# Optimization experiments

Measured on AMD Instinct MI355X. Metric: run time of the kernel, lower is better.

Reference implementation:

```python
import jax, jax.numpy as jnp
import numpy as np

B, C, T = 8, 512, 1024
EXP = 2
E = EXP * C          # 1024, gate/value width
H, HD = 8, 64        # heads, qk head dim
QK = H * HD          # 512
AVG_LEN = 512
EPS = 1e-5


def setup_inputs() -> dict:
    key = jax.random.key(0)
    ks = jax.random.split(key, 10)
    s = 0.02
    return {
        "x": jax.random.normal(ks[0], (B, C, T), jnp.float32),
        "W_in": jax.random.normal(ks[1], (2 * E, C), jnp.float32) * s,
        "b_in": jnp.zeros((2 * E,), jnp.float32),
        "W_attn": jax.random.normal(ks[2], (QK, C), jnp.float32) * s,
        "b_attn": jnp.zeros((QK,), jnp.float32),
        "w_q": 1.0 + jax.random.normal(ks[3], (QK,), jnp.float32) * 0.1,
        "b_q": jax.random.normal(ks[4], (QK,), jnp.float32) * 0.1,
        "w_k": 1.0 + jax.random.normal(ks[5], (QK,), jnp.float32) * 0.1,
        "b_k": jax.random.normal(ks[6], (QK,), jnp.float32) * 0.1,
        "W_out": jax.random.normal(ks[7], (C, E), jnp.float32) * s,
        "b_out": jnp.zeros((C,), jnp.float32),
        "gamma": jnp.ones((C,), jnp.float32),
    }


def reference(x, W_in, b_in, W_attn, b_attn, w_q, b_q, w_k, b_k, W_out, b_out, gamma):
    residual = x
    # mlp_in (1x1 conv) + SiLU, then chunk into gate u and value v, each (B,E,T)
    uv = jax.nn.silu(jnp.einsum('oc,bct->bot', W_in, x) + b_in[:, None])
    u, v = uv[:, :E], uv[:, E:]
    # mlp_attn (1x1 conv); no activation (activation_attn unused in forward)
    z = jnp.einsum('oc,bct->bot', W_attn, x) + b_attn[:, None]  # (B,QK,T)
    # depthwise 1x1 conv on cat(z,z) = two independent per-channel affines
    q = z * w_q[:, None] + b_q[:, None]
    k = z * w_k[:, None] + b_k[:, None]
    # split heads: q,k -> (B,H,T,HD); v -> (B,H,T,E//H)
    q = q.reshape(B, H, HD, T).transpose(0, 1, 3, 2)
    k = k.reshape(B, H, HD, T).transpose(0, 1, 3, 2)
    vh = v.reshape(B, H, E // H, T).transpose(0, 1, 3, 2)
    # entropy-invariant scale: (log n / log avg_len) / sqrt(d)
    scale = (np.log(T) / np.log(AVG_LEN)) / np.sqrt(HD)
    scores = jnp.einsum('bhqd,bhkd->bhqk', q, k) * jnp.float32(scale)
    attn = jax.nn.softmax(scores, axis=-1)
    o = jnp.einsum('bhqk,bhke->bhqe', attn, vh)        # (B,H,T,E//H)
    o = o.transpose(0, 1, 3, 2).reshape(B, E, T)       # back to (B,E,T)
    # gate, project out, residual + RMSNorm over channel dim
    out = jnp.einsum('ce,bet->bct', W_out, u * o) + b_out[:, None]
    y = residual + out
    rms = jax.lax.rsqrt(jnp.mean(y * y, axis=1, keepdims=True) + EPS)
    return y * rms * gamma[:, None]
```

## Files before the change

kernel.cpp:

```cpp
#include <hip/hip_runtime.h>

typedef __attribute__((ext_vector_type(8))) short short8;
typedef __attribute__((ext_vector_type(4))) float f32x4;
typedef __attribute__((ext_vector_type(16))) float f32x16;

__device__ __forceinline__ unsigned short f2b(float f) {
  union { float f; unsigned u; } x; x.f = f;
  unsigned r = (x.u + 0x7fffu + ((x.u >> 16) & 1u)) >> 16;
  return (unsigned short)r;
}
__device__ __forceinline__ float b2f(unsigned short b) {
  union { unsigned u; float f; } x; x.u = ((unsigned)b) << 16;
  return x.f;
}
__device__ __forceinline__ unsigned cvtpk(float lo, float hi) {
  unsigned r;
  asm("v_cvt_pk_bf16_f32 %0, %1, %2" : "=v"(r) : "v"(lo), "v"(hi));
  return r;
}
__device__ __forceinline__ void plswap(unsigned& a, unsigned& b) {
  asm volatile("v_permlane32_swap_b32 %0, %1" : "+v"(a), "+v"(b));
}

#define GLDS16(gp, lp)                                                                  \
  __builtin_amdgcn_global_load_lds((const __attribute__((address_space(1))) void*)(gp), \
                                   (__attribute__((address_space(3))) void*)(lp), 16, 0, 0)

__global__ void prep_w_kernel(const float* __restrict__ W_in, const float* __restrict__ W_attn,
                              const float* __restrict__ W_out, unsigned short* __restrict__ Wcat,
                              unsigned short* __restrict__ WoutB) {
  const int n1 = 2048 * 512, n2 = 512 * 512, n3 = 512 * 1024;
  for (int i = blockIdx.x * 256 + threadIdx.x; i < n1 + n2 + n3; i += gridDim.x * 256) {
    if (i < n1) Wcat[i] = f2b(W_in[i]);
    else if (i < n1 + n2) Wcat[i] = f2b(W_attn[i - n1]);
    else WoutB[i - n1 - n2] = f2b(W_out[i - n1 - n2]);
  }
}

__global__ __launch_bounds__(256) void transpose_x_kernel(const float* __restrict__ x,
                                                          unsigned short* __restrict__ xT) {
  __shared__ float tile[32][33];
  const int bid = blockIdx.x;
  const int b = bid >> 9;
  const int rem = bid & 511;
  const int c0 = (rem >> 5) << 5;
  const int t0 = (rem & 31) << 5;
  const int tj = threadIdx.x & 31, ti = threadIdx.x >> 5;
#pragma unroll
  for (int r = 0; r < 32; r += 8)
    tile[ti + r][tj] = x[(((size_t)b << 9) + c0 + ti + r) * 1024 + t0 + tj];
  __syncthreads();
#pragma unroll
  for (int r = 0; r < 32; r += 8)
    xT[(((size_t)b << 10) + t0 + ti + r) * 512 + c0 + tj] = f2b(tile[tj][ti + r]);
}

__device__ __forceinline__ void gemm_stage(const unsigned short* Ag, const unsigned short* Bg,
                                           int lda, int ldb, int k0, unsigned short* lsA,
                                           unsigned short* lsB, int buf, int sr, int sk,
                                           int ldst) {
  const int bb = buf * 8192;
  GLDS16(Ag + (size_t)sr * lda + k0 + sk, (char*)lsA + bb + ldst);
  GLDS16(Ag + (size_t)(sr + 64) * lda + k0 + sk, (char*)lsA + bb + 4096 + ldst);
  GLDS16(Bg + (size_t)sr * ldb + k0 + sk, (char*)lsB + bb + ldst);
  GLDS16(Bg + (size_t)(sr + 64) * ldb + k0 + sk, (char*)lsB + bb + 4096 + ldst);
}

__device__ __forceinline__ void gemm_bt_core(const unsigned short* __restrict__ Ag,
                                             const unsigned short* __restrict__ Bg, int lda,
                                             int ldb, int K, unsigned short* lsA,
                                             unsigned short* lsB, f32x4 acc[4][4]) {
  const int tid = threadIdx.x;
  const int lane = tid & 63;
  const int w = tid >> 6;
  const int wr = w >> 1, wc = w & 1;
  const int sr = tid >> 2;
  const int sk = (tid & 3) << 3;
  const int ldst = (tid >> 6) << 10;

  const int nt = K >> 5;
  gemm_stage(Ag, Bg, lda, ldb, 0, lsA, lsB, 0, sr, sk, ldst);
  for (int t = 0; t < nt; ++t) {
    const int cur = t & 1;
    if (t + 1 < nt) {
      gemm_stage(Ag, Bg, lda, ldb, (t + 1) << 5, lsA, lsB, cur ^ 1, sr, sk, ldst);
      asm volatile("s_waitcnt vmcnt(4)" ::: "memory");
    } else {
      asm volatile("s_waitcnt vmcnt(0)" ::: "memory");
    }
    __builtin_amdgcn_s_barrier();
    short8 af[4], bfr[4];
    const int bb = cur * 8192;
    const int ko = (lane >> 4) << 4;
    const int ra = (wr << 6) + (lane & 15);
    const int rb = (wc << 6) + (lane & 15);
#pragma unroll
    for (int mi = 0; mi < 4; ++mi)
      af[mi] = *(const short8*)((const char*)lsA + bb + ((ra + (mi << 4)) << 6) + ko);
#pragma unroll
    for (int ni = 0; ni < 4; ++ni)
      bfr[ni] = *(const short8*)((const char*)lsB + bb + ((rb + (ni << 4)) << 6) + ko);
#pragma unroll
    for (int mi = 0; mi < 4; ++mi)
#pragma unroll
      for (int ni = 0; ni < 4; ++ni)
        acc[mi][ni] =
            __builtin_amdgcn_mfma_f32_16x16x32_bf16(af[mi], bfr[ni], acc[mi][ni], 0, 0, 0);
    __builtin_amdgcn_s_barrier();
  }
}

__global__ __launch_bounds__(256) void gemm_a_kernel(
    const unsigned short* __restrict__ Wcat, const unsigned short* __restrict__ xT,
    const float* __restrict__ b_in, const float* __restrict__ b_attn,
    const float* __restrict__ w_q, const float* __restrict__ b_q, const float* __restrict__ w_k,
    const float* __restrict__ b_k, unsigned short* __restrict__ u, unsigned short* __restrict__ v,
    unsigned short* __restrict__ qT, unsigned short* __restrict__ kT) {
  __shared__ __align__(16) unsigned short lsA[16384];
  __shared__ __align__(16) unsigned short lsB[16384];
  const int bid = ((blockIdx.x & 7) * 160) + (blockIdx.x >> 3);
  const int b = bid / 160;
  const int rem = bid % 160;
  const int m0 = (rem >> 3) << 7;
  const int n0 = (rem & 7) << 7;
  f32x4 acc[4][4];
  const f32x4 z4 = {0.f, 0.f, 0.f, 0.f};
#pragma unroll
  for (int mi = 0; mi < 4; ++mi)
#pragma unroll
    for (int ni = 0; ni < 4; ++ni) acc[mi][ni] = z4;

  const unsigned short* Ag = Wcat + (size_t)m0 * 512;
  const unsigned short* Bg = xT + ((size_t)b << 19) + ((size_t)n0 << 9);
  gemm_bt_core(Ag, Bg, 512, 512, 512, lsA, lsB, acc);

  const int lane = threadIdx.x & 63;
  const int w = threadIdx.x >> 6;
  const int wr = w >> 1, wc = w & 1;
#pragma unroll
  for (int mi = 0; mi < 4; ++mi) {
    const int row0 = m0 + (wr << 6) + (mi << 4) + ((lane >> 4) << 2);
#pragma unroll
    for (int ni = 0; ni < 4; ++ni) {
      const int col = n0 + (wc << 6) + (ni << 4) + (lane & 15);
      if (row0 < 2048) {
#pragma unroll
        for (int i = 0; i < 4; ++i) {
          const int row = row0 + i;
          const float s = acc[mi][ni][i] + b_in[row];
          const float r = s / (1.f + __expf(-s));
          if (row < 1024)
            u[((((size_t)b << 10) + row) << 10) + col] = f2b(r);
          else
            v[((((size_t)b << 10) + (row - 1024)) << 10) + col] = f2b(r);
        }
      } else {
        const int c0 = row0 - 2048;
        ushort4 qv, kv;
        unsigned short* qp = (unsigned short*)&qv;
        unsigned short* kp = (unsigned short*)&kv;
#pragma unroll
        for (int i = 0; i < 4; ++i) {
          const int c = c0 + i;
          const float z = acc[mi][ni][i] + b_attn[c];
          qp[i] = f2b(z * w_q[c] + b_q[c]);
          kp[i] = f2b(z * w_k[c] + b_k[c]);
        }
        const int h = c0 >> 6, d = c0 & 63;
        const size_t base = ((((size_t)b * 8 + h) << 10) + col) * 64 + d;
        *(ushort4*)(qT + base) = qv;
        *(ushort4*)(kT + base) = kv;
      }
    }
  }
}

__global__ __launch_bounds__(512, 4) void attn_kernel(const unsigned short* __restrict__ qT,
                                                      const unsigned short* __restrict__ kT,
                                                      const unsigned short* __restrict__ v,
                                                      const unsigned short* __restrict__ u,
                                                      unsigned short* __restrict__ uoT) {
  __shared__ __align__(16) unsigned short Kls[2][4096];
  __shared__ __align__(16) unsigned short Vls[2][8192];
  const float SCALE = 0.13888888888888889f;
  const int bx = blockIdx.x;
  const int xcd = bx & 7, idx = bx >> 3;
  const int bh = (xcd << 3) + (idx & 7);
  const int qb = idx >> 3;
  const int b = bh >> 3, h = bh & 7;
  const int tid = threadIdx.x;
  const int lane = tid & 63;
  const int w = tid >> 6;
  const int l5 = lane >> 5;
  const int l31 = lane & 31;
  const int qw = w >> 1, eh = w & 1;
  const int q0 = qb << 7;

  const unsigned short* qh = qT + ((size_t)bh << 16);
  const unsigned short* kh = kT + ((size_t)bh << 16);
  const unsigned short* vh = v + ((((size_t)b << 10) + (h << 7)) << 10);

  short8 qf[4];
#pragma unroll
  for (int ds = 0; ds < 4; ++ds)
    qf[ds] = *(const short8*)(qh + (size_t)(q0 + (qw << 5) + l31) * 64 + (ds << 4) + (l5 << 3));

  f32x16 o[2];
#pragma unroll
  for (int eb = 0; eb < 2; ++eb)
#pragma unroll
    for (int i = 0; i < 16; ++i) o[eb][i] = 0.f;
  float lacc = 0.f;

  const int srow = tid >> 3;
  const int scol = (((tid & 7) ^ (srow & 7)) << 3);

#define ATTN_STAGE(buf, kt)                                                        \
  {                                                                                \
    const int t2 = (kt) << 6;                                                      \
    GLDS16(kh + (size_t)(t2 + srow) * 64 + scol, (char*)Kls[buf] + (w << 10));     \
    GLDS16(vh + ((size_t)srow << 10) + t2 + scol, (char*)Vls[buf] + (w << 10));    \
    GLDS16(vh + ((size_t)(64 + srow) << 10) + t2 + scol,                           \
           (char*)Vls[buf] + 8192 + (w << 10));                                    \
  }

  ATTN_STAGE(0, 0);
  union U8 { short8 s8; unsigned u4[4]; };
  for (int kt = 0; kt < 16; ++kt) {
    const int cur = kt & 1;
    if (kt < 15) {
      ATTN_STAGE(cur ^ 1, kt + 1);
      asm volatile("s_waitcnt vmcnt(3)" ::: "memory");
    } else {
      asm volatile("s_waitcnt vmcnt(0)" ::: "memory");
    }
    __builtin_amdgcn_s_barrier();

    const char* kb = (const char*)Kls[cur];
    const char* vb = (const char*)Vls[cur];
    U8 pf[4];

    {
      f32x16 s;
#pragma unroll
      for (int i = 0; i < 16; ++i) s[i] = 0.f;
      const int kr = l31;
      __builtin_amdgcn_s_setprio(1);
#pragma unroll
      for (int ds = 0; ds < 4; ++ds) {
        short8 kf = *(const short8*)(kb + (kr << 7) +
                                     (((ds << 5) + (l5 << 4)) ^ ((kr & 7) << 4)));
        s = __builtin_amdgcn_mfma_f32_32x32x16_bf16(kf, qf[ds], s, 0, 0, 0);
      }
      __builtin_amdgcn_s_setprio(0);
      float p[16];
#pragma unroll
      for (int i = 0; i < 16; ++i) {
        p[i] = __expf(s[i] * SCALE);
        lacc += p[i];
      }
      unsigned W00 = cvtpk(p[0], p[1]), W01 = cvtpk(p[2], p[3]);
      unsigned W10 = cvtpk(p[4], p[5]), W11 = cvtpk(p[6], p[7]);
      unsigned W20 = cvtpk(p[8], p[9]), W21 = cvtpk(p[10], p[11]);
      unsigned W30 = cvtpk(p[12], p[13]), W31 = cvtpk(p[14], p[15]);
      unsigned a = W10, bq = W00; plswap(a, bq);
      pf[0].u4[0] = bq; pf[0].u4[2] = a;
      unsigned c = W11, d = W01; plswap(c, d);
      pf[0].u4[1] = d; pf[0].u4[3] = c;
      unsigned e = W30, f = W20; plswap(e, f);
      pf[1].u4[0] = f; pf[1].u4[2] = e;
      unsigned g = W31, hh = W21; plswap(g, hh);
      pf[1].u4[1] = hh; pf[1].u4[3] = g;
    }
    {
      f32x16 s;
#pragma unroll
      for (int i = 0; i < 16; ++i) s[i] = 0.f;
      const int kr = 32 + l31;
      __builtin_amdgcn_s_setprio(1);
#pragma unroll
      for (int ds = 0; ds < 4; ++ds) {
        short8 kf = *(const short8*)(kb + (kr << 7) +
                                     (((ds << 5) + (l5 << 4)) ^ ((kr & 7) << 4)));
        s = __builtin_amdgcn_mfma_f32_32x32x16_bf16(kf, qf[ds], s, 0, 0, 0);
      }
      __builtin_amdgcn_s_setprio(0);
      float p[16];
#pragma unroll
      for (int i = 0; i < 16; ++i) {
        p[i] = __expf(s[i] * SCALE);
        lacc += p[i];
      }
      unsigned W00 = cvtpk(p[0], p[1]), W01 = cvtpk(p[2], p[3]);
      unsigned W10 = cvtpk(p[4], p[5]), W11 = cvtpk(p[6], p[7]);
      unsigned W20 = cvtpk(p[8], p[9]), W21 = cvtpk(p[10], p[11]);
      unsigned W30 = cvtpk(p[12], p[13]), W31 = cvtpk(p[14], p[15]);
      unsigned a = W10, bq = W00; plswap(a, bq);
      pf[2].u4[0] = bq; pf[2].u4[2] = a;
      unsigned c = W11, d = W01; plswap(c, d);
      pf[2].u4[1] = d; pf[2].u4[3] = c;
      unsigned e = W30, f = W20; plswap(e, f);
      pf[3].u4[0] = f; pf[3].u4[2] = e;
      unsigned g = W31, hh = W21; plswap(g, hh);
      pf[3].u4[1] = hh; pf[3].u4[3] = g;
    }

    __builtin_amdgcn_s_setprio(1);
#pragma unroll
    for (int eb = 0; eb < 2; ++eb) {
      const int vrow = (eh << 6) + (eb << 5) + l31;
#pragma unroll
      for (int ks = 0; ks < 4; ++ks) {
        short8 vf = *(const short8*)(vb + (vrow << 7) +
                                     (((ks << 5) + (l5 << 4)) ^ ((vrow & 7) << 4)));
        o[eb] = __builtin_amdgcn_mfma_f32_32x32x16_bf16(vf, pf[ks].s8, o[eb], 0, 0, 0);
      }
    }
    __builtin_amdgcn_s_setprio(0);
    __builtin_amdgcn_s_barrier();
  }
#undef ATTN_STAGE

  lacc += __shfl_xor(lacc, 32, 64);
  const float rl = 1.f / lacc;
  const int t = q0 + (qw << 5) + l31;

#pragma unroll
  for (int eb = 0; eb < 2; ++eb) {
#pragma unroll
    for (int a = 0; a < 4; ++a) {
      const int e4 = (eh << 6) + (eb << 5) + (a << 3) + (l5 << 2);
      const int eg = (h << 7) + e4;
      ushort4 outv;
      unsigned short* op = (unsigned short*)&outv;
#pragma unroll
      for (int j = 0; j < 4; ++j) {
        const int i = (a << 2) + j;
        const float oo = o[eb][i] * rl;
        const float uu = b2f(u[((((size_t)b << 10) + eg + j) << 10) + t]);
        op[j] = f2b(oo * uu);
      }
      *(ushort4*)(uoT + ((((size_t)b << 10) + t) << 10) + eg) = outv;
    }
  }
}

__global__ __launch_bounds__(256) void gemm_c_kernel(const unsigned short* __restrict__ uoT,
                                                     const unsigned short* __restrict__ WoutB,
                                                     const float* __restrict__ x,
                                                     const float* __restrict__ b_out,
                                                     float* __restrict__ y) {
  __shared__ __align__(16) unsigned short lsA[16384];
  __shared__ __align__(16) unsigned short lsB[16384];
  const int bid = ((blockIdx.x & 7) * 32) + (blockIdx.x >> 3);
  const int b = bid >> 5;
  const int rem = bid & 31;
  const int m0 = (rem >> 2) << 7;
  const int n0 = (rem & 3) << 7;
  f32x4 acc[4][4];
  const f32x4 z4 = {0.f, 0.f, 0.f, 0.f};
#pragma unroll
  for (int mi = 0; mi < 4; ++mi)
#pragma unroll
    for (int ni = 0; ni < 4; ++ni) acc[mi][ni] = z4;

  const unsigned short* Ag = uoT + ((size_t)b << 20) + ((size_t)m0 << 10);
  const unsigned short* Bg = WoutB + ((size_t)n0 << 10);
  gemm_bt_core(Ag, Bg, 1024, 1024, 1024, lsA, lsB, acc);

  const int lane = threadIdx.x & 63;
  const int w = threadIdx.x >> 6;
  const int wr = w >> 1, wc = w & 1;
#pragma unroll
  for (int mi = 0; mi < 4; ++mi) {
    const int t4 = m0 + (wr << 6) + (mi << 4) + ((lane >> 4) << 2);
#pragma unroll
    for (int ni = 0; ni < 4; ++ni) {
      const int c = n0 + (wc << 6) + (ni << 4) + (lane & 15);
      const size_t base = ((((size_t)b << 9) + c) << 10) + t4;
      const f32x4 xv = *(const f32x4*)(x + base);
      const float bo = b_out[c];
      f32x4 o;
#pragma unroll
      for (int i = 0; i < 4; ++i) o[i] = acc[mi][ni][i] + bo + xv[i];
      *(f32x4*)(y + base) = o;
    }
  }
}

__global__ __launch_bounds__(256) void rms_kernel(const float* __restrict__ y,
                                                  const float* __restrict__ gamma,
                                                  float* __restrict__ out) {
  __shared__ float part[8][32];
  __shared__ float rmsv[32];
  const int bid = blockIdx.x;
  const int b = bid >> 5;
  const int t0 = (bid & 31) << 5;
  const int tid = threadIdx.x;
  const int tt = tid & 31, cg = tid >> 5;
  const int t = t0 + tt;
  float vals[64];
  float ss = 0.f;
#pragma unroll
  for (int ci = 0; ci < 64; ++ci) {
    const int c = (cg << 6) + ci;
    const float vv = y[((((size_t)b << 9) + c) << 10) + t];
    vals[ci] = vv;
    ss += vv * vv;
  }
  part[cg][tt] = ss;
  __syncthreads();
  if (tid < 32) {
    float tot = 0.f;
#pragma unroll
    for (int g = 0; g < 8; ++g) tot += part[g][tid];
    rmsv[tid] = rsqrtf(tot / 512.f + 1e-5f);
  }
  __syncthreads();
  const float rm = rmsv[tt];
#pragma unroll
  for (int ci = 0; ci < 64; ++ci) {
    const int c = (cg << 6) + ci;
    out[((((size_t)b << 9) + c) << 10) + t] = vals[ci] * rm * gamma[c];
  }
}

extern "C" void kernel_launch(void* const* d_in, const int* in_sizes, int n_in, void* d_out,
                              int out_size, void* d_ws, size_t ws_size, hipStream_t stream) {
  const float* x = (const float*)d_in[0];
  const float* W_in = (const float*)d_in[1];
  const float* b_in = (const float*)d_in[2];
  const float* W_attn = (const float*)d_in[3];
  const float* b_attn = (const float*)d_in[4];
  const float* w_q = (const float*)d_in[5];
  const float* b_q = (const float*)d_in[6];
  const float* w_k = (const float*)d_in[7];
  const float* b_k = (const float*)d_in[8];
  const float* W_out = (const float*)d_in[9];
  const float* b_out = (const float*)d_in[10];
  const float* gamma = (const float*)d_in[11];
  float* out = (float*)d_out;

  char* ws = (char*)d_ws;
  size_t off = 0;
  auto alloc = [&](size_t bytes) {
    char* p = ws + off;
    off += (bytes + 255) & ~(size_t)255;
    return p;
  };
  unsigned short* Wcat = (unsigned short*)alloc((size_t)2560 * 512 * 2);
  unsigned short* WoutB = (unsigned short*)alloc((size_t)512 * 1024 * 2);
  unsigned short* xT = (unsigned short*)alloc((size_t)8 * 1024 * 512 * 2);
  unsigned short* u = (unsigned short*)alloc((size_t)8 * 1024 * 1024 * 2);
  unsigned short* v = (unsigned short*)alloc((size_t)8 * 1024 * 1024 * 2);
  unsigned short* qT = (unsigned short*)alloc((size_t)8 * 8 * 1024 * 64 * 2);
  unsigned short* kT = (unsigned short*)alloc((size_t)8 * 8 * 1024 * 64 * 2);
  unsigned short* uoT = (unsigned short*)alloc((size_t)8 * 1024 * 1024 * 2);
  float* y = (float*)alloc((size_t)8 * 512 * 1024 * 4);
  if (off > ws_size) return;

  prep_w_kernel<<<896, 256, 0, stream>>>(W_in, W_attn, W_out, Wcat, WoutB);
  transpose_x_kernel<<<4096, 256, 0, stream>>>(x, xT);
  gemm_a_kernel<<<1280, 256, 0, stream>>>(Wcat, xT, b_in, b_attn, w_q, b_q, w_k, b_k, u, v, qT,
                                          kT);
  attn_kernel<<<512, 512, 0, stream>>>(qT, kT, v, u, uoT);
  gemm_c_kernel<<<256, 256, 0, stream>>>(uoT, WoutB, x, b_out, y);
  rms_kernel<<<256, 256, 0, stream>>>(y, gamma, out);
}
```

Before: 145.4 us.

## Widen gemm_a tile to 128x256 with 512 threads and trim LDS buffers

The input-projection GEMM now uses 512-thread blocks, each computing a 128x256 output tile with a 2x4 wave layout. Each 256-column tile sits inside one batch, so 640 blocks cover all outputs instead of 1280, and every weight tile loaded from global memory is reused across twice as many columns. The shared buffers are resized to match, and gemm_c's LDS arrays are shrunk to the 16 KB each that gemm_bt_core actually uses, which could raise occupancy. The cost is fewer blocks in flight for gemm_a and a different load and wait pattern per stage.

```diff
diff --git a/kernel.cpp b/kernel.cpp
--- a/kernel.cpp
+++ b/kernel.cpp
@@ -55,74 +55,28 @@
     xT[(((size_t)b << 10) + t0 + ti + r) * 512 + c0 + tj] = f2b(tile[tj][ti + r]);
 }
 
-__device__ __forceinline__ void gemm_stage(const unsigned short* Ag, const unsigned short* Bg,
-                                           int lda, int ldb, int k0, unsigned short* lsA,
-                                           unsigned short* lsB, int buf, int sr, int sk,
-                                           int ldst) {
-  const int bb = buf * 8192;
-  GLDS16(Ag + (size_t)sr * lda + k0 + sk, (char*)lsA + bb + ldst);
-  GLDS16(Ag + (size_t)(sr + 64) * lda + k0 + sk, (char*)lsA + bb + 4096 + ldst);
-  GLDS16(Bg + (size_t)sr * ldb + k0 + sk, (char*)lsB + bb + ldst);
-  GLDS16(Bg + (size_t)(sr + 64) * ldb + k0 + sk, (char*)lsB + bb + 4096 + ldst);
-}
-
-__device__ __forceinline__ void gemm_bt_core(const unsigned short* __restrict__ Ag,
-                                             const unsigned short* __restrict__ Bg, int lda,
-                                             int ldb, int K, unsigned short* lsA,
-                                             unsigned short* lsB, f32x4 acc[4][4]) {
-  const int tid = threadIdx.x;
-  const int lane = tid & 63;
-  const int w = tid >> 6;
-  const int wr = w >> 1, wc = w & 1;
-  const int sr = tid >> 2;
-  const int sk = (tid & 3) << 3;
-  const int ldst = (tid >> 6) << 10;
-
-  const int nt = K >> 5;
-  gemm_stage(Ag, Bg, lda, ldb, 0, lsA, lsB, 0, sr, sk, ldst);
-  for (int t = 0; t < nt; ++t) {
-    const int cur = t & 1;
-    if (t + 1 < nt) {
-      gemm_stage(Ag, Bg, lda, ldb, (t + 1) << 5, lsA, lsB, cur ^ 1, sr, sk, ldst);
-      asm volatile("s_waitcnt vmcnt(4)" ::: "memory");
-    } else {
-      asm volatile("s_waitcnt vmcnt(0)" ::: "memory");
-    }
-    __builtin_amdgcn_s_barrier();
-    short8 af[4], bfr[4];
-    const int bb = cur * 8192;
-    const int ko = (lane >> 4) << 4;
-    const int ra = (wr << 6) + (lane & 15);
-    const int rb = (wc << 6) + (lane & 15);
-#pragma unroll
-    for (int mi = 0; mi < 4; ++mi)
-      af[mi] = *(const short8*)((const char*)lsA + bb + ((ra + (mi << 4)) << 6) + ko);
-#pragma unroll
-    for (int ni = 0; ni < 4; ++ni)
-      bfr[ni] = *(const short8*)((const char*)lsB + bb + ((rb + (ni << 4)) << 6) + ko);
-#pragma unroll
-    for (int mi = 0; mi < 4; ++mi)
-#pragma unroll
-      for (int ni = 0; ni < 4; ++ni)
-        acc[mi][ni] =
-            __builtin_amdgcn_mfma_f32_16x16x32_bf16(af[mi], bfr[ni], acc[mi][ni], 0, 0, 0);
-    __builtin_amdgcn_s_barrier();
-  }
-}
-
-__global__ __launch_bounds__(256) void gemm_a_kernel(
+__global__ __launch_bounds__(512) void gemm_a_kernel(
     const unsigned short* __restrict__ Wcat, const unsigned short* __restrict__ xT,
     const float* __restrict__ b_in, const float* __restrict__ b_attn,
     const float* __restrict__ w_q, const float* __restrict__ b_q, const float* __restrict__ w_k,
     const float* __restrict__ b_k, unsigned short* __restrict__ u, unsigned short* __restrict__ v,
     unsigned short* __restrict__ qT, unsigned short* __restrict__ kT) {
-  __shared__ __align__(16) unsigned short lsA[16384];
+  __shared__ __align__(16) unsigned short lsA[8192];
   __shared__ __align__(16) unsigned short lsB[16384];
-  const int bid = ((blockIdx.x & 7) * 160) + (blockIdx.x >> 3);
-  const int b = bid / 160;
-  const int rem = bid % 160;
-  const int m0 = (rem >> 3) << 7;
-  const int n0 = (rem & 7) << 7;
+  const int lb = ((blockIdx.x & 7) * 80) + (blockIdx.x >> 3);
+  const int n_tile = lb / 20;
+  const int m_tile = lb % 20;
+  const int tid = threadIdx.x;
+  const int lane = tid & 63;
+  const int w = tid >> 6;
+  const int wr = w >> 2, wc = w & 3;
+  const int sr = tid >> 2;
+  const int sk = (tid & 3) << 3;
+  const int ldst = w << 10;
+
+  const unsigned short* Ag = Wcat + (size_t)m_tile * 128 * 512;
+  const unsigned short* Bg = xT + ((size_t)n_tile << 8) * 512;
+
   f32x4 acc[4][4];
   const f32x4 z4 = {0.f, 0.f, 0.f, 0.f};
 #pragma unroll
@@ -130,19 +84,52 @@
 #pragma unroll
     for (int ni = 0; ni < 4; ++ni) acc[mi][ni] = z4;
 
-  const unsigned short* Ag = Wcat + (size_t)m0 * 512;
-  const unsigned short* Bg = xT + ((size_t)b << 19) + ((size_t)n0 << 9);
-  gemm_bt_core(Ag, Bg, 512, 512, 512, lsA, lsB, acc);
-
-  const int lane = threadIdx.x & 63;
-  const int w = threadIdx.x >> 6;
-  const int wr = w >> 1, wc = w & 1;
+#define GA_STAGE(buf, k0)                                                          \
+  {                                                                                \
+    GLDS16(Ag + (size_t)sr * 512 + (k0) + sk, (char*)lsA + (buf)*8192 + ldst);     \
+    GLDS16(Bg + (size_t)sr * 512 + (k0) + sk, (char*)lsB + (buf)*16384 + ldst);    \
+    GLDS16(Bg + (size_t)(128 + sr) * 512 + (k0) + sk,                              \
+           (char*)lsB + (buf)*16384 + 8192 + ldst);                                \
+  }
+
+  GA_STAGE(0, 0);
+  for (int t = 0; t < 16; ++t) {
+    const int cur = t & 1;
+    if (t < 15) {
+      GA_STAGE(cur ^ 1, (t + 1) << 5);
+      asm volatile("s_waitcnt vmcnt(3)" ::: "memory");
+    } else {
+      asm volatile("s_waitcnt vmcnt(0)" ::: "memory");
+    }
+    __builtin_amdgcn_s_barrier();
+    short8 af[4], bfr[4];
+    const int ko = (lane >> 4) << 4;
+    const int ra = (wr << 6) + (lane & 15);
+    const int rb = (wc << 6) + (lane & 15);
+#pragma unroll
+    for (int mi = 0; mi < 4; ++mi)
+      af[mi] = *(const short8*)((const char*)lsA + cur * 8192 + ((ra + (mi << 4)) << 6) + ko);
+#pragma unroll
+    for (int ni = 0; ni < 4; ++ni)
+      bfr[ni] = *(const short8*)((const char*)lsB + cur * 16384 + ((rb + (ni << 4)) << 6) + ko);
+#pragma unroll
+    for (int mi = 0; mi < 4; ++mi)
+#pragma unroll
+      for (int ni = 0; ni < 4; ++ni)
+        acc[mi][ni] =
+            __builtin_amdgcn_mfma_f32_16x16x32_bf16(af[mi], bfr[ni], acc[mi][ni], 0, 0, 0);
+    __builtin_amdgcn_s_barrier();
+  }
+#undef GA_STAGE
+
+  const int b = n_tile >> 2;
+  const int t_base = (n_tile & 3) << 8;
 #pragma unroll
   for (int mi = 0; mi < 4; ++mi) {
-    const int row0 = m0 + (wr << 6) + (mi << 4) + ((lane >> 4) << 2);
+    const int row0 = m_tile * 128 + (wr << 6) + (mi << 4) + ((lane >> 4) << 2);
 #pragma unroll
     for (int ni = 0; ni < 4; ++ni) {
-      const int col = n0 + (wc << 6) + (ni << 4) + (lane & 15);
+      const int col = t_base + (wc << 6) + (ni << 4) + (lane & 15);
       if (row0 < 2048) {
 #pragma unroll
         for (int i = 0; i < 4; ++i) {
@@ -172,6 +159,61 @@
         *(ushort4*)(kT + base) = kv;
       }
     }
+  }
+}
+
+__device__ __forceinline__ void gemm_stage(const unsigned short* Ag, const unsigned short* Bg,
+                                           int lda, int ldb, int k0, unsigned short* lsA,
+                                           unsigned short* lsB, int buf, int sr, int sk,
+                                           int ldst) {
+  const int bb = buf * 8192;
+  GLDS16(Ag + (size_t)sr * lda + k0 + sk, (char*)lsA + bb + ldst);
+  GLDS16(Ag + (size_t)(sr + 64) * lda + k0 + sk, (char*)lsA + bb + 4096 + ldst);
+  GLDS16(Bg + (size_t)sr * ldb + k0 + sk, (char*)lsB + bb + ldst);
+  GLDS16(Bg + (size_t)(sr + 64) * ldb + k0 + sk, (char*)lsB + bb + 4096 + ldst);
+}
+
+__device__ __forceinline__ void gemm_bt_core(const unsigned short* __restrict__ Ag,
+                                             const unsigned short* __restrict__ Bg, int lda,
+                                             int ldb, int K, unsigned short* lsA,
+                                             unsigned short* lsB, f32x4 acc[4][4]) {
+  const int tid = threadIdx.x;
+  const int lane = tid & 63;
+  const int w = tid >> 6;
+  const int wr = w >> 1, wc = w & 1;
+  const int sr = tid >> 2;
+  const int sk = (tid & 3) << 3;
+  const int ldst = (tid >> 6) << 10;
+
+  const int nt = K >> 5;
+  gemm_stage(Ag, Bg, lda, ldb, 0, lsA, lsB, 0, sr, sk, ldst);
+  for (int t = 0; t < nt; ++t) {
+    const int cur = t & 1;
+    if (t + 1 < nt) {
+      gemm_stage(Ag, Bg, lda, ldb, (t + 1) << 5, lsA, lsB, cur ^ 1, sr, sk, ldst);
+      asm volatile("s_waitcnt vmcnt(4)" ::: "memory");
+    } else {
+      asm volatile("s_waitcnt vmcnt(0)" ::: "memory");
+    }
+    __builtin_amdgcn_s_barrier();
+    short8 af[4], bfr[4];
+    const int bb = cur * 8192;
+    const int ko = (lane >> 4) << 4;
+    const int ra = (wr << 6) + (lane & 15);
+    const int rb = (wc << 6) + (lane & 15);
+#pragma unroll
+    for (int mi = 0; mi < 4; ++mi)
+      af[mi] = *(const short8*)((const char*)lsA + bb + ((ra + (mi << 4)) << 6) + ko);
+#pragma unroll
+    for (int ni = 0; ni < 4; ++ni)
+      bfr[ni] = *(const short8*)((const char*)lsB + bb + ((rb + (ni << 4)) << 6) + ko);
+#pragma unroll
+    for (int mi = 0; mi < 4; ++mi)
+#pragma unroll
+      for (int ni = 0; ni < 4; ++ni)
+        acc[mi][ni] =
+            __builtin_amdgcn_mfma_f32_16x16x32_bf16(af[mi], bfr[ni], acc[mi][ni], 0, 0, 0);
+    __builtin_amdgcn_s_barrier();
   }
 }
 
@@ -350,8 +392,8 @@
                                                      const float* __restrict__ x,
                                                      const float* __restrict__ b_out,
                                                      float* __restrict__ y) {
-  __shared__ __align__(16) unsigned short lsA[16384];
-  __shared__ __align__(16) unsigned short lsB[16384];
+  __shared__ __align__(16) unsigned short lsA[8192];
+  __shared__ __align__(16) unsigned short lsB[8192];
   const int bid = ((blockIdx.x & 7) * 32) + (blockIdx.x >> 3);
   const int b = bid >> 5;
   const int rem = bid & 31;
@@ -461,8 +503,8 @@
 
   prep_w_kernel<<<896, 256, 0, stream>>>(W_in, W_attn, W_out, Wcat, WoutB);
   transpose_x_kernel<<<4096, 256, 0, stream>>>(x, xT);
-  gemm_a_kernel<<<1280, 256, 0, stream>>>(Wcat, xT, b_in, b_attn, w_q, b_q, w_k, b_k, u, v, qT,
-                                          kT);
+  gemm_a_kernel<<<640, 512, 0, stream>>>(Wcat, xT, b_in, b_attn, w_q, b_q, w_k, b_k, u, v, qT,
+                                         kT);
   attn_kernel<<<512, 512, 0, stream>>>(qT, kT, v, u, uoT);
   gemm_c_kernel<<<256, 256, 0, stream>>>(uoT, WoutB, x, b_out, y);
   rms_kernel<<<256, 256, 0, stream>>>(y, gamma, out);
```

New measurement: 146.0 us. Within noise of the previous version (+0.4%).

## Rewrite input GEMM to load operands directly into registers with 32x32 MFMA

Applied to the files above, without the earlier changes.

The input-projection GEMM drops its shared-memory staging and barriers. Each wave now loads A and B fragments straight from global memory into registers, double-buffered, and issues 32x32x16 bf16 MFMAs on a larger 128x256 block tile with half as many blocks. The epilogue is adapted to the 32x32 accumulator layout. The output GEMM's shared buffers are halved to their actual double-buffer footprint, which is meant to raise occupancy. The risk is lost cross-wave data reuse through LDS, so more global/L2 traffic and more register pressure per wave.

```diff
diff --git a/kernel.cpp b/kernel.cpp
--- a/kernel.cpp
+++ b/kernel.cpp
@@ -53,6 +53,127 @@
 #pragma unroll
   for (int r = 0; r < 32; r += 8)
     xT[(((size_t)b << 10) + t0 + ti + r) * 512 + c0 + tj] = f2b(tile[tj][ti + r]);
+}
+
+__global__ __launch_bounds__(256, 2) void gemm_a_kernel(
+    const unsigned short* __restrict__ Wcat, const unsigned short* __restrict__ xT,
+    const float* __restrict__ b_in, const float* __restrict__ b_attn,
+    const float* __restrict__ w_q, const float* __restrict__ b_q, const float* __restrict__ w_k,
+    const float* __restrict__ b_k, unsigned short* __restrict__ u, unsigned short* __restrict__ v,
+    unsigned short* __restrict__ qT, unsigned short* __restrict__ kT) {
+  const int lb = ((blockIdx.x & 7) * 80) + (blockIdx.x >> 3);
+  const int n_tile = lb / 20;
+  const int m_tile = lb % 20;
+  const int lane = threadIdx.x & 63;
+  const int w = threadIdx.x >> 6;
+  const int l5 = lane >> 5, l31 = lane & 31;
+  const int mw = m_tile * 128 + (w >> 1) * 64;
+  const int nw = n_tile * 256 + (w & 1) * 128;
+
+  const unsigned short* A0 = Wcat + (size_t)(mw + l31) * 512 + (l5 << 3);
+  const unsigned short* A1 = A0 + 32 * 512;
+  const unsigned short* B0 = xT + (size_t)(nw + l31) * 512 + (l5 << 3);
+  const unsigned short* B1 = B0 + 32 * 512;
+  const unsigned short* B2 = B0 + 64 * 512;
+  const unsigned short* B3 = B0 + 96 * 512;
+
+  f32x16 acc[2][4];
+#pragma unroll
+  for (int mi = 0; mi < 2; ++mi)
+#pragma unroll
+    for (int ni = 0; ni < 4; ++ni)
+#pragma unroll
+      for (int i = 0; i < 16; ++i) acc[mi][ni][i] = 0.f;
+
+  short8 aP[2][2], bP[4][2], aQ[2][2], bQ[4][2];
+
+#define LDA(dst, t)                                     \
+  {                                                     \
+    dst[0][0] = *(const short8*)(A0 + ((t) << 5));      \
+    dst[0][1] = *(const short8*)(A0 + ((t) << 5) + 16); \
+    dst[1][0] = *(const short8*)(A1 + ((t) << 5));      \
+    dst[1][1] = *(const short8*)(A1 + ((t) << 5) + 16); \
+  }
+#define LDB(dst, t)                                     \
+  {                                                     \
+    dst[0][0] = *(const short8*)(B0 + ((t) << 5));      \
+    dst[0][1] = *(const short8*)(B0 + ((t) << 5) + 16); \
+    dst[1][0] = *(const short8*)(B1 + ((t) << 5));      \
+    dst[1][1] = *(const short8*)(B1 + ((t) << 5) + 16); \
+    dst[2][0] = *(const short8*)(B2 + ((t) << 5));      \
+    dst[2][1] = *(const short8*)(B2 + ((t) << 5) + 16); \
+    dst[3][0] = *(const short8*)(B3 + ((t) << 5));      \
+    dst[3][1] = *(const short8*)(B3 + ((t) << 5) + 16); \
+  }
+#define CALC(a_, b_)                                                                   \
+  {                                                                                    \
+    _Pragma("unroll") for (int mi = 0; mi < 2; ++mi) _Pragma("unroll") for (int ni = 0; \
+                                                                            ni < 4;    \
+                                                                            ++ni)      \
+        _Pragma("unroll") for (int kk = 0; kk < 2; ++kk) acc[mi][ni] =                 \
+            __builtin_amdgcn_mfma_f32_32x32x16_bf16(a_[mi][kk], b_[ni][kk],            \
+                                                    acc[mi][ni], 0, 0, 0);             \
+  }
+
+  LDA(aP, 0);
+  LDB(bP, 0);
+  for (int i = 0; i < 7; ++i) {
+    LDA(aQ, 2 * i + 1);
+    LDB(bQ, 2 * i + 1);
+    CALC(aP, bP);
+    LDA(aP, 2 * i + 2);
+    LDB(bP, 2 * i + 2);
+    CALC(aQ, bQ);
+  }
+  LDA(aQ, 15);
+  LDB(bQ, 15);
+  CALC(aP, bP);
+  CALC(aQ, bQ);
+#undef LDA
+#undef LDB
+#undef CALC
+
+  const int b = n_tile >> 2;
+  const int tcol_base = (n_tile & 3) * 256 + (w & 1) * 128;
+#pragma unroll
+  for (int mi = 0; mi < 2; ++mi) {
+#pragma unroll
+    for (int ni = 0; ni < 4; ++ni) {
+      const int col = tcol_base + ni * 32 + l31;
+#pragma unroll
+      for (int g = 0; g < 4; ++g) {
+        const int row0 = mw + mi * 32 + (g << 3) + (l5 << 2);
+        if (row0 < 2048) {
+#pragma unroll
+          for (int j = 0; j < 4; ++j) {
+            const int row = row0 + j;
+            const float s = acc[mi][ni][(g << 2) + j] + b_in[row];
+            const float r = s / (1.f + __expf(-s));
+            if (row < 1024)
+              u[((((size_t)b << 10) + row) << 10) + col] = f2b(r);
+            else
+              v[((((size_t)b << 10) + (row - 1024)) << 10) + col] = f2b(r);
+          }
+        } else {
+          const int c0 = row0 - 2048;
+          ushort4 qv, kv;
+          unsigned short* qp = (unsigned short*)&qv;
+          unsigned short* kp = (unsigned short*)&kv;
+#pragma unroll
+          for (int j = 0; j < 4; ++j) {
+            const int c = c0 + j;
+            const float z = acc[mi][ni][(g << 2) + j] + b_attn[c];
+            qp[j] = f2b(z * w_q[c] + b_q[c]);
+            kp[j] = f2b(z * w_k[c] + b_k[c]);
+          }
+          const int h = c0 >> 6, d = c0 & 63;
+          const size_t base = ((((size_t)b * 8 + h) << 10) + col) * 64 + d;
+          *(ushort4*)(qT + base) = qv;
+          *(ushort4*)(kT + base) = kv;
+        }
+      }
+    }
+  }
 }
 
 __device__ __forceinline__ void gemm_stage(const unsigned short* Ag, const unsigned short* Bg,
@@ -107,71 +228,6 @@
         acc[mi][ni] =
             __builtin_amdgcn_mfma_f32_16x16x32_bf16(af[mi], bfr[ni], acc[mi][ni], 0, 0, 0);
     __builtin_amdgcn_s_barrier();
-  }
-}
-
-__global__ __launch_bounds__(256) void gemm_a_kernel(
-    const unsigned short* __restrict__ Wcat, const unsigned short* __restrict__ xT,
-    const float* __restrict__ b_in, const float* __restrict__ b_attn,
-    const float* __restrict__ w_q, const float* __restrict__ b_q, const float* __restrict__ w_k,
-    const float* __restrict__ b_k, unsigned short* __restrict__ u, unsigned short* __restrict__ v,
-    unsigned short* __restrict__ qT, unsigned short* __restrict__ kT) {
-  __shared__ __align__(16) unsigned short lsA[16384];
-  __shared__ __align__(16) unsigned short lsB[16384];
-  const int bid = ((blockIdx.x & 7) * 160) + (blockIdx.x >> 3);
-  const int b = bid / 160;
-  const int rem = bid % 160;
-  const int m0 = (rem >> 3) << 7;
-  const int n0 = (rem & 7) << 7;
-  f32x4 acc[4][4];
-  const f32x4 z4 = {0.f, 0.f, 0.f, 0.f};
-#pragma unroll
-  for (int mi = 0; mi < 4; ++mi)
-#pragma unroll
-    for (int ni = 0; ni < 4; ++ni) acc[mi][ni] = z4;
-
-  const unsigned short* Ag = Wcat + (size_t)m0 * 512;
-  const unsigned short* Bg = xT + ((size_t)b << 19) + ((size_t)n0 << 9);
-  gemm_bt_core(Ag, Bg, 512, 512, 512, lsA, lsB, acc);
-
-  const int lane = threadIdx.x & 63;
-  const int w = threadIdx.x >> 6;
-  const int wr = w >> 1, wc = w & 1;
-#pragma unroll
-  for (int mi = 0; mi < 4; ++mi) {
-    const int row0 = m0 + (wr << 6) + (mi << 4) + ((lane >> 4) << 2);
-#pragma unroll
-    for (int ni = 0; ni < 4; ++ni) {
-      const int col = n0 + (wc << 6) + (ni << 4) + (lane & 15);
-      if (row0 < 2048) {
-#pragma unroll
-        for (int i = 0; i < 4; ++i) {
-          const int row = row0 + i;
-          const float s = acc[mi][ni][i] + b_in[row];
-          const float r = s / (1.f + __expf(-s));
-          if (row < 1024)
-            u[((((size_t)b << 10) + row) << 10) + col] = f2b(r);
-          else
-            v[((((size_t)b << 10) + (row - 1024)) << 10) + col] = f2b(r);
-        }
-      } else {
-        const int c0 = row0 - 2048;
-        ushort4 qv, kv;
-        unsigned short* qp = (unsigned short*)&qv;
-        unsigned short* kp = (unsigned short*)&kv;
-#pragma unroll
-        for (int i = 0; i < 4; ++i) {
-          const int c = c0 + i;
-          const float z = acc[mi][ni][i] + b_attn[c];
-          qp[i] = f2b(z * w_q[c] + b_q[c]);
-          kp[i] = f2b(z * w_k[c] + b_k[c]);
-        }
-        const int h = c0 >> 6, d = c0 & 63;
-        const size_t base = ((((size_t)b * 8 + h) << 10) + col) * 64 + d;
-        *(ushort4*)(qT + base) = qv;
-        *(ushort4*)(kT + base) = kv;
-      }
-    }
   }
 }
 
@@ -350,8 +406,8 @@
                                                      const float* __restrict__ x,
                                                      const float* __restrict__ b_out,
                                                      float* __restrict__ y) {
-  __shared__ __align__(16) unsigned short lsA[16384];
-  __shared__ __align__(16) unsigned short lsB[16384];
+  __shared__ __align__(16) unsigned short lsA[8192];
+  __shared__ __align__(16) unsigned short lsB[8192];
   const int bid = ((blockIdx.x & 7) * 32) + (blockIdx.x >> 3);
   const int b = bid >> 5;
   const int rem = bid & 31;
@@ -461,8 +517,8 @@
 
   prep_w_kernel<<<896, 256, 0, stream>>>(W_in, W_attn, W_out, Wcat, WoutB);
   transpose_x_kernel<<<4096, 256, 0, stream>>>(x, xT);
-  gemm_a_kernel<<<1280, 256, 0, stream>>>(Wcat, xT, b_in, b_attn, w_q, b_q, w_k, b_k, u, v, qT,
-                                          kT);
+  gemm_a_kernel<<<640, 256, 0, stream>>>(Wcat, xT, b_in, b_attn, w_q, b_q, w_k, b_k, u, v, qT,
+                                         kT);
   attn_kernel<<<512, 512, 0, stream>>>(qT, kT, v, u, uoT);
   gemm_c_kernel<<<256, 256, 0, stream>>>(uoT, WoutB, x, b_out, y);
   rms_kernel<<<256, 256, 0, stream>>>(y, gamma, out);
```

Measured after the change: 185.2 us. +27.3%, slower.
